# Kernel tuning notes

Measured on AMD Instinct MI355X. Metric: run time of the kernel, lower is better.

The kernel has to match this reference:

```python
import jax, jax.numpy as jnp
import numpy as np


def setup_inputs() -> dict:
    key = jax.random.key(0)
    k1, k2, k3 = jax.random.split(key, 3)
    B, H, F, O = 2048, 512, 128, 10
    inputs = jax.random.normal(k1, (B, F), dtype=jnp.float32)
    # centers ~ uniform(-1, 1) as in init_params
    centers = jax.random.uniform(k2, (H, F), dtype=jnp.float32, minval=-1.0, maxval=1.0)
    sigma = jnp.ones((1,), dtype=jnp.float32)
    W = jax.random.normal(k3, (O, H), dtype=jnp.float32) * (1.0 / np.sqrt(H))
    b = jnp.zeros((O,), dtype=jnp.float32)
    return {"inputs": inputs, "centers": centers, "sigma": sigma, "W": W, "b": b}


def reference(inputs, centers, sigma, W, b):
    # pairwise squared distances: [B, H, F] diff -> sum over F -> [B, H]
    diff = inputs[:, None, :] - centers[None, :, :]
    distances = jnp.sum(diff * diff, axis=-1)  # [B, H]
    rbf = jnp.exp(-distances / (2.0 * sigma[0] ** 2))  # [B, H]
    # linear: y = rbf @ W.T + b
    return rbf @ W.T + b
```

## Files before the change

kernel.cpp:

```cpp
#include <hip/hip_runtime.h>


constexpr int Fdim = 128;
constexpr int Hdim = 512;
constexpr int Odim = 10;
constexpr int BM   = 8;
constexpr int KC   = 16;
constexpr int NCH  = Fdim / KC;
constexpr int LDXT = 12;

__global__ __launch_bounds__(512, 1) void rbf_all(
    const float* __restrict__ x,
    const float* __restrict__ c,
    const float* __restrict__ sigmap,
    const float* __restrict__ W,
    const float* __restrict__ bias,
    float* __restrict__ out)
{
    __shared__ float c_s[2][KC][Hdim];
    __shared__ float xT[Fdim][LDXT];
    __shared__ float rbf_s[BM][Hdim];
    __shared__ float cn_s[Hdim];
    __shared__ float po_s[BM][8][Odim];
    __shared__ float xn_s[BM];

    const int tid  = threadIdx.x;
    const int lane = tid & 63;
    const int wave = tid >> 6;
    const int wr   = wave >> 2;
    const int wh   = wave & 3;
    const int row0 = blockIdx.x * BM;

    const float4* x4 = reinterpret_cast<const float4*>(x);
    const float4* c4 = reinterpret_cast<const float4*>(c);

    const int sfq = tid & 3;
    const int sh  = tid >> 2;

    float4 pre[4];
    float cnp[4] = {0.0f, 0.0f, 0.0f, 0.0f};

#define CLOAD(k)                                                              \
    {                                                                         \
        _Pragma("unroll")                                                     \
        for (int p = 0; p < 4; ++p)                                           \
            pre[p] = c4[(size_t)(sh + 128 * p) * (Fdim / 4) + (k) * 4 + sfq]; \
    }
#define CWRITE(k)                                                             \
    {                                                                         \
        _Pragma("unroll")                                                     \
        for (int p = 0; p < 4; ++p) {                                         \
            float4 v = pre[p];                                                \
            int h = sh + 128 * p;                                             \
            c_s[(k) & 1][4 * sfq + 0][h] = v.x;                               \
            c_s[(k) & 1][4 * sfq + 1][h] = v.y;                               \
            c_s[(k) & 1][4 * sfq + 2][h] = v.z;                               \
            c_s[(k) & 1][4 * sfq + 3][h] = v.w;                               \
            cnp[p] += v.x * v.x + v.y * v.y + v.z * v.z + v.w * v.w;          \
        }                                                                     \
    }

    CLOAD(0);

    if (tid < 256) {
        int r  = tid >> 5;
        int fq = tid & 31;
        float4 v = x4[(size_t)(row0 + r) * (Fdim / 4) + fq];
        xT[4 * fq + 0][r] = v.x;
        xT[4 * fq + 1][r] = v.y;
        xT[4 * fq + 2][r] = v.z;
        xT[4 * fq + 3][r] = v.w;
        float s = v.x * v.x + v.y * v.y + v.z * v.z + v.w * v.w;
#pragma unroll
        for (int sft = 1; sft < 32; sft <<= 1) s += __shfl_xor(s, sft, 64);
        if (fq == 0) xn_s[r] = s;
    }

    CWRITE(0);
    CLOAD(1);
    __syncthreads();

    float acc[4][2];
#pragma unroll
    for (int i = 0; i < 4; ++i) { acc[i][0] = 0.0f; acc[i][1] = 0.0f; }

    for (int k = 0; k < NCH; ++k) {
#pragma unroll
        for (int f = 0; f < KC; ++f) {
            float4 xv = *reinterpret_cast<const float4*>(&xT[k * KC + f][4 * wr]);
            float2 cv = *reinterpret_cast<const float2*>(
                &c_s[k & 1][f][wh * 128 + 2 * lane]);
            acc[0][0] = fmaf(xv.x, cv.x, acc[0][0]);
            acc[0][1] = fmaf(xv.x, cv.y, acc[0][1]);
            acc[1][0] = fmaf(xv.y, cv.x, acc[1][0]);
            acc[1][1] = fmaf(xv.y, cv.y, acc[1][1]);
            acc[2][0] = fmaf(xv.z, cv.x, acc[2][0]);
            acc[2][1] = fmaf(xv.z, cv.y, acc[2][1]);
            acc[3][0] = fmaf(xv.w, cv.x, acc[3][0]);
            acc[3][1] = fmaf(xv.w, cv.y, acc[3][1]);
        }
        if (k + 1 < NCH) {
            CWRITE(k + 1);
            if (k + 2 < NCH) CLOAD(k + 2);
            __syncthreads();
        }
    }
#undef CLOAD
#undef CWRITE

    float2 W2[Odim][4];
#pragma unroll
    for (int o = 0; o < Odim; ++o)
#pragma unroll
        for (int kk = 0; kk < 4; ++kk)
            W2[o][kk] = *reinterpret_cast<const float2*>(
                &W[o * Hdim + 2 * lane + 128 * kk]);

#pragma unroll
    for (int p = 0; p < 4; ++p) {
        float s = cnp[p];
        s += __shfl_xor(s, 1, 64);
        s += __shfl_xor(s, 2, 64);
        cnp[p] = s;
    }
    if (sfq == 0) {
#pragma unroll
        for (int p = 0; p < 4; ++p) cn_s[sh + 128 * p] = cnp[p];
    }
    __syncthreads();

    const float sg    = sigmap[0];
    const float scale = -1.0f / (2.0f * sg * sg);
    {
        float2 cn = *reinterpret_cast<const float2*>(&cn_s[wh * 128 + 2 * lane]);
#pragma unroll
        for (int i = 0; i < 4; ++i) {
            float xn = xn_s[4 * wr + i];
            float2 rv;
            rv.x = __expf((xn + cn.x - 2.0f * acc[i][0]) * scale);
            rv.y = __expf((xn + cn.y - 2.0f * acc[i][1]) * scale);
            *reinterpret_cast<float2*>(&rbf_s[4 * wr + i][wh * 128 + 2 * lane]) = rv;
        }
    }
    __syncthreads();

    {
        const int row = wave;
        float po[Odim];
#pragma unroll
        for (int o = 0; o < Odim; ++o) po[o] = 0.0f;

#pragma unroll
        for (int kk = 0; kk < 4; ++kk) {
            float2 rv = *reinterpret_cast<const float2*>(
                &rbf_s[row][2 * lane + 128 * kk]);
#pragma unroll
            for (int o = 0; o < Odim; ++o) {
                po[o] = fmaf(rv.x, W2[o][kk].x, po[o]);
                po[o] = fmaf(rv.y, W2[o][kk].y, po[o]);
            }
        }
#pragma unroll
        for (int s = 1; s < 8; s <<= 1) {
#pragma unroll
            for (int o = 0; o < Odim; ++o)
                po[o] += __shfl_xor(po[o], s, 64);
        }
        if ((lane & 7) == 0) {
#pragma unroll
            for (int o = 0; o < Odim; ++o)
                po_s[row][lane >> 3][o] = po[o];
        }
    }
    __syncthreads();

    if (tid < BM * Odim) {
        int w = tid / Odim;
        int o = tid - w * Odim;
        float v = bias[o];
#pragma unroll
        for (int g = 0; g < 8; ++g) v += po_s[w][g][o];
        out[(size_t)(row0 + w) * Odim + o] = v;
    }
}

extern "C" void kernel_launch(void* const* d_in, const int* in_sizes, int n_in,
                              void* d_out, int out_size, void* d_ws, size_t ws_size,
                              hipStream_t stream) {
    const float* x  = (const float*)d_in[0];
    const float* c  = (const float*)d_in[1];
    const float* sg = (const float*)d_in[2];
    const float* W  = (const float*)d_in[3];
    const float* b  = (const float*)d_in[4];
    float* out      = (float*)d_out;

    const int B = in_sizes[0] / Fdim;

    rbf_all<<<B / BM, 512, 0, stream>>>(x, c, sg, W, b, out);
}
```

Baseline: 19.16 us.

## Halve rows per block, single-buffer padded centers tile, raise occupancy

Each block now handles 4 batch rows instead of 8, doubling the grid to 512 blocks. The centers tile becomes a single padded buffer, adding an extra barrier per chunk, and launch bounds now allow 4 blocks per CU. Each thread computes one hidden unit for 4 rows rather than 2 units, and the output projection splits each row across two waves. The aim is more parallelism and occupancy with less shared memory per block. The cost is that every block re-reads the full centers matrix from global memory twice as often overall, loses double-buffering, and does less reuse per thread.

```diff
diff --git a/kernel.cpp b/kernel.cpp
--- a/kernel.cpp
+++ b/kernel.cpp
@@ -4,12 +4,14 @@
 constexpr int Fdim = 128;
 constexpr int Hdim = 512;
 constexpr int Odim = 10;
-constexpr int BM   = 8;
+constexpr int BM   = 4;
 constexpr int KC   = 16;
 constexpr int NCH  = Fdim / KC;
-constexpr int LDXT = 12;
+constexpr int LDC  = 513;
+constexpr int LDXT = 8;
+constexpr int LDR  = 516;
 
-__global__ __launch_bounds__(512, 1) void rbf_all(
+__global__ __launch_bounds__(512, 4) void rbf_all(
     const float* __restrict__ x,
     const float* __restrict__ c,
     const float* __restrict__ sigmap,
@@ -17,18 +19,16 @@
     const float* __restrict__ bias,
     float* __restrict__ out)
 {
-    __shared__ float c_s[2][KC][Hdim];
+    __shared__ float cT[KC][LDC];
     __shared__ float xT[Fdim][LDXT];
-    __shared__ float rbf_s[BM][Hdim];
+    __shared__ float rbf_s[BM][LDR];
+    __shared__ float po_s[BM][16][Odim];
+    __shared__ float xn_s[BM];
     __shared__ float cn_s[Hdim];
-    __shared__ float po_s[BM][8][Odim];
-    __shared__ float xn_s[BM];
 
     const int tid  = threadIdx.x;
     const int lane = tid & 63;
     const int wave = tid >> 6;
-    const int wr   = wave >> 2;
-    const int wh   = wave & 3;
     const int row0 = blockIdx.x * BM;
 
     const float4* x4 = reinterpret_cast<const float4*>(x);
@@ -40,29 +40,29 @@
     float4 pre[4];
     float cnp[4] = {0.0f, 0.0f, 0.0f, 0.0f};
 
-#define CLOAD(k)                                                              \
-    {                                                                         \
-        _Pragma("unroll")                                                     \
-        for (int p = 0; p < 4; ++p)                                           \
-            pre[p] = c4[(size_t)(sh + 128 * p) * (Fdim / 4) + (k) * 4 + sfq]; \
+#define CLOAD(k)                                                               \
+    {                                                                          \
+        _Pragma("unroll")                                                      \
+        for (int p = 0; p < 4; ++p)                                            \
+            pre[p] = c4[(size_t)(sh + 128 * p) * (Fdim / 4) + (k) * 4 + sfq];  \
     }
-#define CWRITE(k)                                                             \
-    {                                                                         \
-        _Pragma("unroll")                                                     \
-        for (int p = 0; p < 4; ++p) {                                         \
-            float4 v = pre[p];                                                \
-            int h = sh + 128 * p;                                             \
-            c_s[(k) & 1][4 * sfq + 0][h] = v.x;                               \
-            c_s[(k) & 1][4 * sfq + 1][h] = v.y;                               \
-            c_s[(k) & 1][4 * sfq + 2][h] = v.z;                               \
-            c_s[(k) & 1][4 * sfq + 3][h] = v.w;                               \
-            cnp[p] += v.x * v.x + v.y * v.y + v.z * v.z + v.w * v.w;          \
-        }                                                                     \
+#define CWRITE(k)                                                              \
+    {                                                                          \
+        _Pragma("unroll")                                                      \
+        for (int p = 0; p < 4; ++p) {                                          \
+            float4 v = pre[p];                                                 \
+            int h = sh + 128 * p;                                              \
+            cT[4 * sfq + 0][h] = v.x;                                          \
+            cT[4 * sfq + 1][h] = v.y;                                          \
+            cT[4 * sfq + 2][h] = v.z;                                          \
+            cT[4 * sfq + 3][h] = v.w;                                          \
+            cnp[p] += v.x * v.x + v.y * v.y + v.z * v.z + v.w * v.w;           \
+        }                                                                      \
     }
 
     CLOAD(0);
 
-    if (tid < 256) {
+    if (tid < 128) {
         int r  = tid >> 5;
         int fq = tid & 31;
         float4 v = x4[(size_t)(row0 + r) * (Fdim / 4) + fq];
@@ -80,26 +80,21 @@
     CLOAD(1);
     __syncthreads();
 
-    float acc[4][2];
-#pragma unroll
-    for (int i = 0; i < 4; ++i) { acc[i][0] = 0.0f; acc[i][1] = 0.0f; }
+    float acc[4] = {0.0f, 0.0f, 0.0f, 0.0f};
+    const int hown = wave * 64 + lane;
 
     for (int k = 0; k < NCH; ++k) {
 #pragma unroll
         for (int f = 0; f < KC; ++f) {
-            float4 xv = *reinterpret_cast<const float4*>(&xT[k * KC + f][4 * wr]);
-            float2 cv = *reinterpret_cast<const float2*>(
-                &c_s[k & 1][f][wh * 128 + 2 * lane]);
-            acc[0][0] = fmaf(xv.x, cv.x, acc[0][0]);
-            acc[0][1] = fmaf(xv.x, cv.y, acc[0][1]);
-            acc[1][0] = fmaf(xv.y, cv.x, acc[1][0]);
-            acc[1][1] = fmaf(xv.y, cv.y, acc[1][1]);
-            acc[2][0] = fmaf(xv.z, cv.x, acc[2][0]);
-            acc[2][1] = fmaf(xv.z, cv.y, acc[2][1]);
-            acc[3][0] = fmaf(xv.w, cv.x, acc[3][0]);
-            acc[3][1] = fmaf(xv.w, cv.y, acc[3][1]);
+            float4 xv = *reinterpret_cast<const float4*>(&xT[k * KC + f][0]);
+            float  cv = cT[f][hown];
+            acc[0] = fmaf(xv.x, cv, acc[0]);
+            acc[1] = fmaf(xv.y, cv, acc[1]);
+            acc[2] = fmaf(xv.z, cv, acc[2]);
+            acc[3] = fmaf(xv.w, cv, acc[3]);
         }
         if (k + 1 < NCH) {
+            __syncthreads();
             CWRITE(k + 1);
             if (k + 2 < NCH) CLOAD(k + 2);
             __syncthreads();
@@ -108,13 +103,15 @@
 #undef CLOAD
 #undef CWRITE
 
-    float2 W2[Odim][4];
+    const int erow  = wave & 3;
+    const int ehalf = wave >> 2;
+    float2 W2[Odim][2];
 #pragma unroll
     for (int o = 0; o < Odim; ++o)
 #pragma unroll
-        for (int kk = 0; kk < 4; ++kk)
+        for (int kk = 0; kk < 2; ++kk)
             W2[o][kk] = *reinterpret_cast<const float2*>(
-                &W[o * Hdim + 2 * lane + 128 * kk]);
+                &W[o * Hdim + ehalf * 256 + 2 * lane + 128 * kk]);
 
 #pragma unroll
     for (int p = 0; p < 4; ++p) {
@@ -132,28 +129,24 @@
     const float sg    = sigmap[0];
     const float scale = -1.0f / (2.0f * sg * sg);
     {
-        float2 cn = *reinterpret_cast<const float2*>(&cn_s[wh * 128 + 2 * lane]);
+        float cn = cn_s[hown];
 #pragma unroll
-        for (int i = 0; i < 4; ++i) {
-            float xn = xn_s[4 * wr + i];
-            float2 rv;
-            rv.x = __expf((xn + cn.x - 2.0f * acc[i][0]) * scale);
-            rv.y = __expf((xn + cn.y - 2.0f * acc[i][1]) * scale);
-            *reinterpret_cast<float2*>(&rbf_s[4 * wr + i][wh * 128 + 2 * lane]) = rv;
+        for (int r = 0; r < 4; ++r) {
+            float d = xn_s[r] + cn - 2.0f * acc[r];
+            rbf_s[r][hown] = __expf(d * scale);
         }
     }
     __syncthreads();
 
     {
-        const int row = wave;
         float po[Odim];
 #pragma unroll
         for (int o = 0; o < Odim; ++o) po[o] = 0.0f;
 
 #pragma unroll
-        for (int kk = 0; kk < 4; ++kk) {
+        for (int kk = 0; kk < 2; ++kk) {
             float2 rv = *reinterpret_cast<const float2*>(
-                &rbf_s[row][2 * lane + 128 * kk]);
+                &rbf_s[erow][ehalf * 256 + 2 * lane + 128 * kk]);
 #pragma unroll
             for (int o = 0; o < Odim; ++o) {
                 po[o] = fmaf(rv.x, W2[o][kk].x, po[o]);
@@ -169,7 +162,7 @@
         if ((lane & 7) == 0) {
 #pragma unroll
             for (int o = 0; o < Odim; ++o)
-                po_s[row][lane >> 3][o] = po[o];
+                po_s[erow][ehalf * 8 + (lane >> 3)][o] = po[o];
         }
     }
     __syncthreads();
@@ -179,7 +172,7 @@
         int o = tid - w * Odim;
         float v = bias[o];
 #pragma unroll
-        for (int g = 0; g < 8; ++g) v += po_s[w][g][o];
+        for (int g = 0; g < 16; ++g) v += po_s[w][g][o];
         out[(size_t)(row0 + w) * Odim + o] = v;
     }
 }
```

Measured after the change: 25.31 us. +32.1%, slower.
